# Performance work log

Hardware: AMD Instinct MI355X
Metric: run time of the kernel (lower is better)

The kernel has to match this reference:

```python
import jax, jax.numpy as jnp
import numpy as np

B, M, P, A, T = 32, 128, 20, 32, 32
H = 32   # embed_size / local hidden
E = 64   # local_hidden_dim = 2*H, global attention embed dim


def setup_inputs() -> dict:
    key = jax.random.key(0)
    ks = jax.random.split(key, 10)
    def w(k, shape, fan):
        return jax.random.normal(k, shape, jnp.float32) / np.float32(np.sqrt(fan))
    z = lambda *s: jnp.zeros(s, jnp.float32)
    o = lambda *s: jnp.ones(s, jnp.float32)
    return {
        "map_states": jax.random.normal(ks[0], (B, M, P, 16), jnp.float32),
        "agent_states": jax.random.normal(ks[1], (B, A, T, 4), jnp.float32),
        "m_W1": w(ks[2], (16, H), 16), "m_b1": z(H), "m_g1": o(H), "m_be1": z(H),
        "m_W2": w(ks[3], (H, H), H),   "m_b2": z(H), "m_g2": o(H), "m_be2": z(H),
        "a_W1": w(ks[4], (4, H), 4),   "a_b1": z(H), "a_g1": o(H), "a_be1": z(H),
        "a_W2": w(ks[5], (H, H), H),   "a_b2": z(H), "a_g2": o(H), "a_be2": z(H),
        # stacked attention params: index 0 = a2m, 1 = agent(self), 2 = m2a
        "att_Wq": w(ks[6], (3, E, E), E), "att_bq": z(3, E),
        "att_Wk": w(ks[7], (3, E, E), E), "att_bk": z(3, E),
        "att_Wv": w(ks[8], (3, E, E), E), "att_bv": z(3, E),
        "att_Wo": w(ks[9], (3, E, E), E), "att_bo": z(3, E),
    }


def _mlp(x, W, b, g, be):
    # Linear -> LayerNorm -> ReLU
    h = x @ W + b
    mu = jnp.mean(h, axis=-1, keepdims=True)
    var = jnp.var(h, axis=-1, keepdims=True)
    h = (h - mu) / jnp.sqrt(var + 1e-5) * g + be
    return jax.nn.relu(h)


def _local_graph(x, p1, p2):
    # x: [B, N, P, F] -> [B, N, 2H]
    e = _mlp(_mlp(x, *p1), *p2)                       # [B,N,P,H]
    n = e.shape[2]
    # faithful "max excluding self": max_j (e[j] - 10000*[j==i])
    mask = -10000.0 * jnp.eye(n, dtype=e.dtype)       # [Pi,Pj]
    nb = jnp.max(e[:, :, None, :, :] + mask[None, None, :, :, None], axis=3)  # [B,N,P,H]
    e = jnp.concatenate([e, nb], axis=-1)             # [B,N,P,2H]
    return jnp.max(e, axis=2)                          # [B,N,2H]


def _mha(q, k, v, Wq, bq, Wk, bk, Wv, bv, Wo, bo):
    # single-head attention, batch_first
    d = q.shape[-1]
    Q = q @ Wq + bq
    K = k @ Wk + bk
    V = v @ Wv + bv
    scores = jnp.einsum('bqd,bkd->bqk', Q, K) / jnp.sqrt(jnp.asarray(d, Q.dtype))
    attn = jax.nn.softmax(scores, axis=-1)
    return jnp.einsum('bqk,bkd->bqd', attn, V) @ Wo + bo


def reference(map_states, agent_states,
              m_W1, m_b1, m_g1, m_be1, m_W2, m_b2, m_g2, m_be2,
              a_W1, a_b1, a_g1, a_be1, a_W2, a_b2, a_g2, a_be2,
              att_Wq, att_bq, att_Wk, att_bk, att_Wv, att_bv, att_Wo, att_bo):
    map_emb = _local_graph(map_states, (m_W1, m_b1, m_g1, m_be1), (m_W2, m_b2, m_g2, m_be2))      # [B,M,E]
    agent_emb = _local_graph(agent_states, (a_W1, a_b1, a_g1, a_be1), (a_W2, a_b2, a_g2, a_be2))  # [B,A,E]

    target = agent_emb[:, :1]                                       # [B,1,E]
    kv = jnp.concatenate([target, map_emb], axis=1)                 # [B,M+1,E]
    a2m = _mha(map_emb, kv, kv, att_Wq[0], att_bq[0], att_Wk[0], att_bk[0],
               att_Wv[0], att_bv[0], att_Wo[0], att_bo[0])
    map_emb = map_emb + a2m
    t_a = _mha(target, target, target, att_Wq[1], att_bq[1], att_Wk[1], att_bk[1],
               att_Wv[1], att_bv[1], att_Wo[1], att_bo[1])
    t_m2a = _mha(target, map_emb, map_emb, att_Wq[2], att_bq[2], att_Wk[2], att_bk[2],
                 att_Wv[2], att_bv[2], att_Wo[2], att_bo[2])
    target = t_a + t_m2a                                            # [B,1,E]
    # pack (target_agent_embedding, map_embedding) into one array [B, M+1, E]
    return jnp.concatenate([target, map_emb], axis=1)
```

## Files before the change

kernel.cpp:

```cpp
#include <hip/hip_runtime.h>

#define BB 32
#define MM 128
#define PP 20
#define AA 32
#define TT 32
#define HH 32
#define EE 64

__device__ __forceinline__ float4 matvec64(const float* __restrict__ W,
                                           const float* __restrict__ xrow,
                                           int s, int t)
{
    const float4* __restrict__ Wv = (const float4*)W;
    const float4* __restrict__ xv = (const float4*)xrow;
    float4 acc = make_float4(0.f, 0.f, 0.f, 0.f);
#pragma unroll
    for (int ii = 0; ii < 4; ++ii) {
        const float4 xx = xv[s * 4 + ii];
        const int ib = s * 16 + ii * 4;
        const float4 w0 = Wv[(ib + 0) * 16 + t];
        const float4 w1 = Wv[(ib + 1) * 16 + t];
        const float4 w2 = Wv[(ib + 2) * 16 + t];
        const float4 w3 = Wv[(ib + 3) * 16 + t];
        acc.x = fmaf(xx.x, w0.x, acc.x); acc.y = fmaf(xx.x, w0.y, acc.y);
        acc.z = fmaf(xx.x, w0.z, acc.z); acc.w = fmaf(xx.x, w0.w, acc.w);
        acc.x = fmaf(xx.y, w1.x, acc.x); acc.y = fmaf(xx.y, w1.y, acc.y);
        acc.z = fmaf(xx.y, w1.z, acc.z); acc.w = fmaf(xx.y, w1.w, acc.w);
        acc.x = fmaf(xx.z, w2.x, acc.x); acc.y = fmaf(xx.z, w2.y, acc.y);
        acc.z = fmaf(xx.z, w2.z, acc.z); acc.w = fmaf(xx.z, w2.w, acc.w);
        acc.x = fmaf(xx.w, w3.x, acc.x); acc.y = fmaf(xx.w, w3.y, acc.y);
        acc.z = fmaf(xx.w, w3.z, acc.z); acc.w = fmaf(xx.w, w3.w, acc.w);
    }
    acc.x += __shfl_xor(acc.x, 16); acc.y += __shfl_xor(acc.y, 16);
    acc.z += __shfl_xor(acc.z, 16); acc.w += __shfl_xor(acc.w, 16);
    acc.x += __shfl_xor(acc.x, 32); acc.y += __shfl_xor(acc.y, 32);
    acc.z += __shfl_xor(acc.z, 32); acc.w += __shfl_xor(acc.w, 32);
    return acc;
}

template <int IN>
__device__ __forceinline__ void lg_body(const float* __restrict__ xg, int P,
                                        const float* __restrict__ W1, const float* __restrict__ b1,
                                        const float* __restrict__ g1, const float* __restrict__ be1,
                                        const float* __restrict__ W2, const float* __restrict__ b2,
                                        const float* __restrict__ g2, const float* __restrict__ be2,
                                        float* __restrict__ outRow)
{
    const int lane = threadIdx.x;
    const int sub  = lane >> 5;
    const int c    = lane & 31;

    float w1c[IN];
#pragma unroll
    for (int k = 0; k < IN; ++k) w1c[k] = W1[k * HH + c];
    float w2c[HH];
#pragma unroll
    for (int k = 0; k < HH; ++k) w2c[k] = W2[k * HH + c];
    const float b1c = b1[c], g1c = g1[c], be1c = be1[c];
    const float b2c = b2[c], g2c = g2[c], be2c = be2[c];

    float cmax = -1e30f;

    for (int p0 = 0; p0 < P; p0 += 2) {
        const int p = p0 + sub;
        const float* xp = xg + (long)p * IN;

        float h = b1c;
#pragma unroll
        for (int k = 0; k < IN; ++k) h = fmaf(xp[k], w1c[k], h);

        float sdot = h;
#pragma unroll
        for (int off = 16; off >= 1; off >>= 1) sdot += __shfl_xor(sdot, off, 32);
        const float mu = sdot * (1.0f / 32.0f);
        float d = h - mu;
        float sq = d * d;
#pragma unroll
        for (int off = 16; off >= 1; off >>= 1) sq += __shfl_xor(sq, off, 32);
        const float var = sq * (1.0f / 32.0f);
        float a = d * rsqrtf(var + 1e-5f) * g1c + be1c;
        a = fmaxf(a, 0.0f);

        float h2 = b2c;
#pragma unroll
        for (int k = 0; k < HH; ++k) h2 = fmaf(__shfl(a, k, 32), w2c[k], h2);

        float s2 = h2;
#pragma unroll
        for (int off = 16; off >= 1; off >>= 1) s2 += __shfl_xor(s2, off, 32);
        const float mu2 = s2 * (1.0f / 32.0f);
        float d2 = h2 - mu2;
        float sq2 = d2 * d2;
#pragma unroll
        for (int off = 16; off >= 1; off >>= 1) sq2 += __shfl_xor(sq2, off, 32);
        const float var2 = sq2 * (1.0f / 32.0f);
        float e = d2 * rsqrtf(var2 + 1e-5f) * g2c + be2c;
        e = fmaxf(e, 0.0f);

        cmax = fmaxf(cmax, e);
    }

    const float other = __shfl_xor(cmax, 32);
    cmax = fmaxf(cmax, other);
    if (sub == 0) {
        outRow[c]      = cmax;
        outRow[32 + c] = cmax;
    }
}

__global__ void lg_fused_kernel(const float* __restrict__ map_states,
                                const float* __restrict__ agent_states,
                                const float* __restrict__ mW1, const float* __restrict__ mb1,
                                const float* __restrict__ mg1, const float* __restrict__ mbe1,
                                const float* __restrict__ mW2, const float* __restrict__ mb2,
                                const float* __restrict__ mg2, const float* __restrict__ mbe2,
                                const float* __restrict__ aW1, const float* __restrict__ ab1,
                                const float* __restrict__ ag1, const float* __restrict__ abe1,
                                const float* __restrict__ aW2, const float* __restrict__ ab2,
                                const float* __restrict__ ag2, const float* __restrict__ abe2,
                                float* __restrict__ map_emb, float* __restrict__ target)
{
    const int g = blockIdx.x;
    if (g < BB * MM) {
        lg_body<16>(map_states + (long)g * PP * 16, PP,
                    mW1, mb1, mg1, mbe1, mW2, mb2, mg2, mbe2,
                    map_emb + (long)g * EE);
    } else {
        const int b = g - BB * MM;
        lg_body<4>(agent_states + (long)b * AA * TT * 4, TT,
                   aW1, ab1, ag1, abe1, aW2, ab2, ag2, abe2,
                   target + (long)b * EE);
    }
}

__global__ void kv_a2m_kernel(const float* __restrict__ map_emb,
                              const float* __restrict__ target,
                              const float* __restrict__ Wk, const float* __restrict__ bk,
                              const float* __restrict__ Wv, const float* __restrict__ bv,
                              float* __restrict__ Kb,
                              float* __restrict__ Vb)
{
    const int blk = blockIdx.x;
    const int b = blk / 129;
    const int r = blk % 129;
    const int lane = threadIdx.x;
    const int s = lane >> 4, t = lane & 15;

    __shared__ __align__(16) float xrow[EE];
    const float* src = (r == 0) ? (target + (long)b * EE)
                                : (map_emb + ((long)b * MM + (r - 1)) * EE);
    xrow[lane] = src[lane];
    __syncthreads();

    const float4 k4 = matvec64(Wk, xrow, s, t);
    const float4 v4 = matvec64(Wv, xrow, s, t);
    if (s == 0) {
        const float4 kb4 = ((const float4*)bk)[t];
        const float4 vb4 = ((const float4*)bv)[t];
        float4 ko, vo;
        ko.x = k4.x + kb4.x; ko.y = k4.y + kb4.y; ko.z = k4.z + kb4.z; ko.w = k4.w + kb4.w;
        vo.x = v4.x + vb4.x; vo.y = v4.y + vb4.y; vo.z = v4.z + vb4.z; vo.w = v4.w + vb4.w;
        ((float4*)(Kb + ((long)b * 129 + r) * EE))[t] = ko;
        ((float4*)(Vb + ((long)b * 129 + r) * EE))[t] = vo;
    }
}

__global__ void attn_fused_kernel(const float* __restrict__ map_emb,
                                  const float* __restrict__ Kb,
                                  const float* __restrict__ Vb,
                                  const float* __restrict__ Wq, const float* __restrict__ bq,
                                  const float* __restrict__ Wo, const float* __restrict__ bo,
                                  const float* __restrict__ Wk2, const float* __restrict__ bk2,
                                  const float* __restrict__ Wv2, const float* __restrict__ bv2,
                                  float* __restrict__ K2,
                                  float* __restrict__ V2,
                                  float* __restrict__ out)
{
    const int blk  = blockIdx.x;
    const int b    = blk >> 7;
    const int q    = blk & 127;
    const int lane = threadIdx.x;
    const int s = lane >> 4, t = lane & 15;

    __shared__ __align__(16) float xrow[EE];
    __shared__ __align__(16) float sc[132];
    __shared__ __align__(16) float av[EE];
    __shared__ __align__(16) float resrow[EE];

    xrow[lane] = map_emb[((long)b * MM + q) * EE + lane];
    __syncthreads();

    float4 q4 = matvec64(Wq, xrow, s, t);
    {
        const float4 bq4 = ((const float4*)bq)[t];
        q4.x = (q4.x + bq4.x) * 0.125f;
        q4.y = (q4.y + bq4.y) * 0.125f;
        q4.z = (q4.z + bq4.z) * 0.125f;
        q4.w = (q4.w + bq4.w) * 0.125f;
    }

    const float* Kbase = Kb + (long)b * 129 * EE;
    float mx = -1e30f;
#pragma unroll 4
    for (int it = 0; it < 33; ++it) {
        const int j = it * 4 + s;
        const bool valid = (j < 129);
        float p = 0.0f;
        if (valid) {
            const float4 k4 = ((const float4*)(Kbase + (long)j * EE))[t];
            p = q4.x * k4.x + q4.y * k4.y + q4.z * k4.z + q4.w * k4.w;
        }
        p += __shfl_xor(p, 1); p += __shfl_xor(p, 2);
        p += __shfl_xor(p, 4); p += __shfl_xor(p, 8);
        if (valid) {
            mx = fmaxf(mx, p);
            if (t == 0) sc[j] = p;
        }
    }
#pragma unroll
    for (int off = 32; off >= 1; off >>= 1) mx = fmaxf(mx, __shfl_xor(mx, off));
    __syncthreads();

    float sum = 0.0f;
    for (int j = lane; j < 129; j += 64) {
        const float e = __expf(sc[j] - mx);
        sc[j] = e;
        sum += e;
    }
#pragma unroll
    for (int off = 32; off >= 1; off >>= 1) sum += __shfl_xor(sum, off);
    const float inv = 1.0f / sum;
    __syncthreads();

    const float* Vbase = Vb + (long)b * 129 * EE;
    float acc = 0.0f;
#pragma unroll 4
    for (int j0 = 0; j0 < 128; j0 += 4) {
        const float4 s4 = *(const float4*)&sc[j0];
        acc = fmaf(s4.x, Vbase[(long)(j0 + 0) * EE + lane], acc);
        acc = fmaf(s4.y, Vbase[(long)(j0 + 1) * EE + lane], acc);
        acc = fmaf(s4.z, Vbase[(long)(j0 + 2) * EE + lane], acc);
        acc = fmaf(s4.w, Vbase[(long)(j0 + 3) * EE + lane], acc);
    }
    acc = fmaf(sc[128], Vbase[(long)128 * EE + lane], acc);
    acc *= inv;
    av[lane] = acc;
    __syncthreads();

    const float4 o4 = matvec64(Wo, av, s, t);
    const float4 bo4 = ((const float4*)bo)[t];
    const float4 x4 = ((const float4*)xrow)[t];
    float4 res;
    res.x = o4.x + bo4.x + x4.x;
    res.y = o4.y + bo4.y + x4.y;
    res.z = o4.z + bo4.z + x4.z;
    res.w = o4.w + bo4.w + x4.w;
    if (s == 0) {
        ((float4*)(out + ((long)b * 129 + 1 + q) * EE))[t] = res;
        ((float4*)resrow)[t] = res;
    }
    __syncthreads();

    const float4 k4 = matvec64(Wk2, resrow, s, t);
    const float4 v4 = matvec64(Wv2, resrow, s, t);
    if (s == 0) {
        const float4 kb4 = ((const float4*)bk2)[t];
        const float4 vb4 = ((const float4*)bv2)[t];
        float4 ko, vo;
        ko.x = k4.x + kb4.x; ko.y = k4.y + kb4.y; ko.z = k4.z + kb4.z; ko.w = k4.w + kb4.w;
        vo.x = v4.x + vb4.x; vo.y = v4.y + vb4.y; vo.z = v4.z + vb4.z; vo.w = v4.w + vb4.w;
        ((float4*)(K2 + ((long)b * MM + q) * EE))[t] = ko;
        ((float4*)(V2 + ((long)b * MM + q) * EE))[t] = vo;
    }
}

__global__ void target_kernel(const float* __restrict__ target,
                              const float* __restrict__ K2, const float* __restrict__ V2,
                              const float* __restrict__ Wq2, const float* __restrict__ bq2,
                              const float* __restrict__ Wo2, const float* __restrict__ bo2,
                              const float* __restrict__ Wv1, const float* __restrict__ bv1,
                              const float* __restrict__ Wo1, const float* __restrict__ bo1,
                              float* __restrict__ out)
{
    const int b    = blockIdx.x;
    const int lane = threadIdx.x;
    const int s = lane >> 4, t = lane & 15;

    __shared__ __align__(16) float trow[EE];
    __shared__ __align__(16) float tmp[EE];
    __shared__ __align__(16) float sc[128];
    __shared__ __align__(16) float av[EE];

    trow[lane] = target[(long)b * EE + lane];
    __syncthreads();

    const float4 v1 = matvec64(Wv1, trow, s, t);
    if (s == 0) {
        const float4 bv4 = ((const float4*)bv1)[t];
        float4 w; w.x = v1.x + bv4.x; w.y = v1.y + bv4.y; w.z = v1.z + bv4.z; w.w = v1.w + bv4.w;
        ((float4*)tmp)[t] = w;
    }
    __syncthreads();
    float4 ta = matvec64(Wo1, tmp, s, t);
    {
        const float4 bo4 = ((const float4*)bo1)[t];
        ta.x += bo4.x; ta.y += bo4.y; ta.z += bo4.z; ta.w += bo4.w;
    }

    float4 q4 = matvec64(Wq2, trow, s, t);
    {
        const float4 bq4 = ((const float4*)bq2)[t];
        q4.x = (q4.x + bq4.x) * 0.125f;
        q4.y = (q4.y + bq4.y) * 0.125f;
        q4.z = (q4.z + bq4.z) * 0.125f;
        q4.w = (q4.w + bq4.w) * 0.125f;
    }

    const float* Kbase = K2 + (long)b * MM * EE;
    float mx = -1e30f;
#pragma unroll 4
    for (int it = 0; it < 32; ++it) {
        const int j = it * 4 + s;
        const float4 k4 = ((const float4*)(Kbase + (long)j * EE))[t];
        float p = q4.x * k4.x + q4.y * k4.y + q4.z * k4.z + q4.w * k4.w;
        p += __shfl_xor(p, 1); p += __shfl_xor(p, 2);
        p += __shfl_xor(p, 4); p += __shfl_xor(p, 8);
        mx = fmaxf(mx, p);
        if (t == 0) sc[j] = p;
    }
#pragma unroll
    for (int off = 32; off >= 1; off >>= 1) mx = fmaxf(mx, __shfl_xor(mx, off));
    __syncthreads();

    float sum = 0.0f;
#pragma unroll
    for (int j = lane; j < MM; j += 64) {
        const float e = __expf(sc[j] - mx);
        sc[j] = e;
        sum += e;
    }
#pragma unroll
    for (int off = 32; off >= 1; off >>= 1) sum += __shfl_xor(sum, off);
    const float inv = 1.0f / sum;
    __syncthreads();

    const float* Vbase = V2 + (long)b * MM * EE;
    float acc = 0.0f;
#pragma unroll 4
    for (int j0 = 0; j0 < 128; j0 += 4) {
        const float4 s4 = *(const float4*)&sc[j0];
        acc = fmaf(s4.x, Vbase[(long)(j0 + 0) * EE + lane], acc);
        acc = fmaf(s4.y, Vbase[(long)(j0 + 1) * EE + lane], acc);
        acc = fmaf(s4.z, Vbase[(long)(j0 + 2) * EE + lane], acc);
        acc = fmaf(s4.w, Vbase[(long)(j0 + 3) * EE + lane], acc);
    }
    acc *= inv;
    av[lane] = acc;
    __syncthreads();

    const float4 o4 = matvec64(Wo2, av, s, t);
    if (s == 0) {
        const float4 bo4 = ((const float4*)bo2)[t];
        float4 r;
        r.x = ta.x + o4.x + bo4.x;
        r.y = ta.y + o4.y + bo4.y;
        r.z = ta.z + o4.z + bo4.z;
        r.w = ta.w + o4.w + bo4.w;
        ((float4*)(out + (long)b * 129 * EE))[t] = r;
    }
}

extern "C" void kernel_launch(void* const* d_in, const int* in_sizes, int n_in,
                              void* d_out, int out_size, void* d_ws, size_t ws_size,
                              hipStream_t stream)
{
    const float* map_states   = (const float*)d_in[0];
    const float* agent_states = (const float*)d_in[1];
    const float* m_W1 = (const float*)d_in[2];
    const float* m_b1 = (const float*)d_in[3];
    const float* m_g1 = (const float*)d_in[4];
    const float* m_be1 = (const float*)d_in[5];
    const float* m_W2 = (const float*)d_in[6];
    const float* m_b2 = (const float*)d_in[7];
    const float* m_g2 = (const float*)d_in[8];
    const float* m_be2 = (const float*)d_in[9];
    const float* a_W1 = (const float*)d_in[10];
    const float* a_b1 = (const float*)d_in[11];
    const float* a_g1 = (const float*)d_in[12];
    const float* a_be1 = (const float*)d_in[13];
    const float* a_W2 = (const float*)d_in[14];
    const float* a_b2 = (const float*)d_in[15];
    const float* a_g2 = (const float*)d_in[16];
    const float* a_be2 = (const float*)d_in[17];
    const float* att_Wq = (const float*)d_in[18];
    const float* att_bq = (const float*)d_in[19];
    const float* att_Wk = (const float*)d_in[20];
    const float* att_bk = (const float*)d_in[21];
    const float* att_Wv = (const float*)d_in[22];
    const float* att_bv = (const float*)d_in[23];
    const float* att_Wo = (const float*)d_in[24];
    const float* att_bo = (const float*)d_in[25];

    float* out = (float*)d_out;

    float* ws      = (float*)d_ws;
    float* map_emb = ws;
    float* target  = map_emb + BB * MM * EE;
    float* Kb      = target + BB * EE;
    float* Vb      = Kb + BB * 129 * EE;
    float* K2      = Vb + BB * 129 * EE;
    float* V2      = K2 + BB * MM * EE;

    const float* Wq0 = att_Wq + 0 * EE * EE; const float* bq0 = att_bq + 0 * EE;
    const float* Wk0 = att_Wk + 0 * EE * EE; const float* bk0 = att_bk + 0 * EE;
    const float* Wv0 = att_Wv + 0 * EE * EE; const float* bv0 = att_bv + 0 * EE;
    const float* Wo0 = att_Wo + 0 * EE * EE; const float* bo0 = att_bo + 0 * EE;
    const float* Wv1 = att_Wv + 1 * EE * EE; const float* bv1 = att_bv + 1 * EE;
    const float* Wo1 = att_Wo + 1 * EE * EE; const float* bo1 = att_bo + 1 * EE;
    const float* Wq2 = att_Wq + 2 * EE * EE; const float* bq2 = att_bq + 2 * EE;
    const float* Wk2 = att_Wk + 2 * EE * EE; const float* bk2 = att_bk + 2 * EE;
    const float* Wv2 = att_Wv + 2 * EE * EE; const float* bv2 = att_bv + 2 * EE;
    const float* Wo2 = att_Wo + 2 * EE * EE; const float* bo2 = att_bo + 2 * EE;

    hipLaunchKernelGGL(lg_fused_kernel, dim3(BB * MM + BB), dim3(64), 0, stream,
                       map_states, agent_states,
                       m_W1, m_b1, m_g1, m_be1, m_W2, m_b2, m_g2, m_be2,
                       a_W1, a_b1, a_g1, a_be1, a_W2, a_b2, a_g2, a_be2,
                       map_emb, target);

    hipLaunchKernelGGL(kv_a2m_kernel, dim3(BB * 129), dim3(64), 0, stream,
                       map_emb, target, Wk0, bk0, Wv0, bv0, Kb, Vb);

    hipLaunchKernelGGL(attn_fused_kernel, dim3(BB * MM), dim3(64), 0, stream,
                       map_emb, Kb, Vb, Wq0, bq0, Wo0, bo0,
                       Wk2, bk2, Wv2, bv2, K2, V2, out);

    hipLaunchKernelGGL(target_kernel, dim3(BB), dim3(64), 0, stream,
                       target, K2, V2, Wq2, bq2, Wo2, bo2, Wv1, bv1, Wo1, bo1, out);
}
```

Baseline: 196.0 us.

## Fuse local-graph encoder with a2m Q/K/V projections and widen blocks to 128 threads

Merges the local-graph embedding kernel with the K/V projection kernel, and moves the Q projection (pre-scaled by 1/sqrt(d)) out of the attention kernel, so each map/agent row's Q, K and V are computed right after its embedding in one launch. Blocks grow to 128 threads, handling 4 points per iteration with a shared-memory cross-wave max. The second MLP layer now broadcasts activations through LDS instead of 32 shuffles, and attention-value accumulations use four independent accumulators. This removes one kernel launch and the re-read of embeddings, at the cost of extra Q-buffer traffic and larger per-block shared memory and syncs.

```diff
diff --git a/kernel.cpp b/kernel.cpp
--- a/kernel.cpp
+++ b/kernel.cpp
@@ -40,16 +40,28 @@
 }
 
 template <int IN>
-__device__ __forceinline__ void lg_body(const float* __restrict__ xg, int P,
-                                        const float* __restrict__ W1, const float* __restrict__ b1,
-                                        const float* __restrict__ g1, const float* __restrict__ be1,
-                                        const float* __restrict__ W2, const float* __restrict__ b2,
-                                        const float* __restrict__ g2, const float* __restrict__ be2,
-                                        float* __restrict__ outRow)
-{
-    const int lane = threadIdx.x;
-    const int sub  = lane >> 5;
-    const int c    = lane & 31;
+__device__ __forceinline__ void lg_qkv_body(const float* __restrict__ xg, int P,
+                                            const float* __restrict__ W1, const float* __restrict__ b1,
+                                            const float* __restrict__ g1, const float* __restrict__ be1,
+                                            const float* __restrict__ W2, const float* __restrict__ b2,
+                                            const float* __restrict__ g2, const float* __restrict__ be2,
+                                            float* __restrict__ embRow,
+                                            const float* __restrict__ Wq, const float* __restrict__ bq,
+                                            const float* __restrict__ Wk, const float* __restrict__ bk,
+                                            const float* __restrict__ Wv, const float* __restrict__ bv,
+                                            float* __restrict__ Qrow,
+                                            float* __restrict__ Krow,
+                                            float* __restrict__ Vrow)
+{
+    const int tid  = threadIdx.x;
+    const int wave = tid >> 6;
+    const int lane = tid & 63;
+    const int sub  = tid >> 5;
+    const int c    = tid & 31;
+
+    __shared__ __align__(16) float aslot[4][32];
+    __shared__ __align__(16) float wmax[2][32];
+    __shared__ __align__(16) float xrow[EE];
 
     float w1c[IN];
 #pragma unroll
@@ -62,13 +74,27 @@
 
     float cmax = -1e30f;
 
-    for (int p0 = 0; p0 < P; p0 += 2) {
+    for (int p0 = 0; p0 < P; p0 += 4) {
         const int p = p0 + sub;
         const float* xp = xg + (long)p * IN;
 
         float h = b1c;
-#pragma unroll
-        for (int k = 0; k < IN; ++k) h = fmaf(xp[k], w1c[k], h);
+        if (IN == 16) {
+            const float4* xp4 = (const float4*)xp;
+            const float4 x0 = xp4[0], x1 = xp4[1], x2 = xp4[2], x3 = xp4[3];
+            h = fmaf(x0.x, w1c[0], h);  h = fmaf(x0.y, w1c[1], h);
+            h = fmaf(x0.z, w1c[2], h);  h = fmaf(x0.w, w1c[3], h);
+            h = fmaf(x1.x, w1c[4], h);  h = fmaf(x1.y, w1c[5], h);
+            h = fmaf(x1.z, w1c[6], h);  h = fmaf(x1.w, w1c[7], h);
+            h = fmaf(x2.x, w1c[8], h);  h = fmaf(x2.y, w1c[9], h);
+            h = fmaf(x2.z, w1c[10], h); h = fmaf(x2.w, w1c[11], h);
+            h = fmaf(x3.x, w1c[12], h); h = fmaf(x3.y, w1c[13], h);
+            h = fmaf(x3.z, w1c[14], h); h = fmaf(x3.w, w1c[15], h);
+        } else {
+            const float4 x0 = *(const float4*)xp;
+            h = fmaf(x0.x, w1c[0], h); h = fmaf(x0.y, w1c[1], h);
+            h = fmaf(x0.z, w1c[2], h); h = fmaf(x0.w, w1c[3], h);
+        }
 
         float sdot = h;
 #pragma unroll
@@ -82,9 +108,17 @@
         float a = d * rsqrtf(var + 1e-5f) * g1c + be1c;
         a = fmaxf(a, 0.0f);
 
+        aslot[sub][c] = a;
+        const float4* av4 = (const float4*)aslot[sub];
         float h2 = b2c;
 #pragma unroll
-        for (int k = 0; k < HH; ++k) h2 = fmaf(__shfl(a, k, 32), w2c[k], h2);
+        for (int j = 0; j < 8; ++j) {
+            const float4 aa = av4[j];
+            h2 = fmaf(aa.x, w2c[4 * j + 0], h2);
+            h2 = fmaf(aa.y, w2c[4 * j + 1], h2);
+            h2 = fmaf(aa.z, w2c[4 * j + 2], h2);
+            h2 = fmaf(aa.w, w2c[4 * j + 3], h2);
+        }
 
         float s2 = h2;
 #pragma unroll
@@ -101,75 +135,98 @@
         cmax = fmaxf(cmax, e);
     }
 
-    const float other = __shfl_xor(cmax, 32);
-    cmax = fmaxf(cmax, other);
-    if (sub == 0) {
-        outRow[c]      = cmax;
-        outRow[32 + c] = cmax;
-    }
-}
-
-__global__ void lg_fused_kernel(const float* __restrict__ map_states,
-                                const float* __restrict__ agent_states,
-                                const float* __restrict__ mW1, const float* __restrict__ mb1,
-                                const float* __restrict__ mg1, const float* __restrict__ mbe1,
-                                const float* __restrict__ mW2, const float* __restrict__ mb2,
-                                const float* __restrict__ mg2, const float* __restrict__ mbe2,
-                                const float* __restrict__ aW1, const float* __restrict__ ab1,
-                                const float* __restrict__ ag1, const float* __restrict__ abe1,
-                                const float* __restrict__ aW2, const float* __restrict__ ab2,
-                                const float* __restrict__ ag2, const float* __restrict__ abe2,
-                                float* __restrict__ map_emb, float* __restrict__ target)
+    cmax = fmaxf(cmax, __shfl_xor(cmax, 32));
+    if (lane < 32) wmax[wave][lane] = cmax;
+    __syncthreads();
+
+    if (tid < 32) {
+        const float fin = fmaxf(wmax[0][tid], wmax[1][tid]);
+        xrow[tid]      = fin;
+        xrow[tid + 32] = fin;
+        embRow[tid]      = fin;
+        embRow[tid + 32] = fin;
+    }
+    __syncthreads();
+
+    const int s = lane >> 4, t = lane & 15;
+    if (wave == 0) {
+        if (Qrow) {
+            float4 q4 = matvec64(Wq, xrow, s, t);
+            if (s == 0) {
+                const float4 bq4 = ((const float4*)bq)[t];
+                float4 qo;
+                qo.x = (q4.x + bq4.x) * 0.125f;
+                qo.y = (q4.y + bq4.y) * 0.125f;
+                qo.z = (q4.z + bq4.z) * 0.125f;
+                qo.w = (q4.w + bq4.w) * 0.125f;
+                ((float4*)Qrow)[t] = qo;
+            }
+        }
+        float4 k4 = matvec64(Wk, xrow, s, t);
+        if (s == 0) {
+            const float4 kb4 = ((const float4*)bk)[t];
+            float4 ko;
+            ko.x = k4.x + kb4.x; ko.y = k4.y + kb4.y;
+            ko.z = k4.z + kb4.z; ko.w = k4.w + kb4.w;
+            ((float4*)Krow)[t] = ko;
+        }
+    } else {
+        float4 v4 = matvec64(Wv, xrow, s, t);
+        if (s == 0) {
+            const float4 vb4 = ((const float4*)bv)[t];
+            float4 vo;
+            vo.x = v4.x + vb4.x; vo.y = v4.y + vb4.y;
+            vo.z = v4.z + vb4.z; vo.w = v4.w + vb4.w;
+            ((float4*)Vrow)[t] = vo;
+        }
+    }
+}
+
+__global__ void lg_qkv_kernel(const float* __restrict__ map_states,
+                              const float* __restrict__ agent_states,
+                              const float* __restrict__ mW1, const float* __restrict__ mb1,
+                              const float* __restrict__ mg1, const float* __restrict__ mbe1,
+                              const float* __restrict__ mW2, const float* __restrict__ mb2,
+                              const float* __restrict__ mg2, const float* __restrict__ mbe2,
+                              const float* __restrict__ aW1, const float* __restrict__ ab1,
+                              const float* __restrict__ ag1, const float* __restrict__ abe1,
+                              const float* __restrict__ aW2, const float* __restrict__ ab2,
+                              const float* __restrict__ ag2, const float* __restrict__ abe2,
+                              const float* __restrict__ Wq, const float* __restrict__ bq,
+                              const float* __restrict__ Wk, const float* __restrict__ bk,
+                              const float* __restrict__ Wv, const float* __restrict__ bv,
+                              float* __restrict__ map_emb,
+                              float* __restrict__ target,
+                              float* __restrict__ Qb,
+                              float* __restrict__ Kb,
+                              float* __restrict__ Vb)
 {
     const int g = blockIdx.x;
     if (g < BB * MM) {
-        lg_body<16>(map_states + (long)g * PP * 16, PP,
-                    mW1, mb1, mg1, mbe1, mW2, mb2, mg2, mbe2,
-                    map_emb + (long)g * EE);
+        const int b = g >> 7, m = g & 127;
+        lg_qkv_body<16>(map_states + (long)g * PP * 16, PP,
+                        mW1, mb1, mg1, mbe1, mW2, mb2, mg2, mbe2,
+                        map_emb + (long)g * EE,
+                        Wq, bq, Wk, bk, Wv, bv,
+                        Qb + (long)g * EE,
+                        Kb + ((long)b * 129 + 1 + m) * EE,
+                        Vb + ((long)b * 129 + 1 + m) * EE);
     } else {
         const int b = g - BB * MM;
-        lg_body<4>(agent_states + (long)b * AA * TT * 4, TT,
-                   aW1, ab1, ag1, abe1, aW2, ab2, ag2, abe2,
-                   target + (long)b * EE);
-    }
-}
-
-__global__ void kv_a2m_kernel(const float* __restrict__ map_emb,
-                              const float* __restrict__ target,
-                              const float* __restrict__ Wk, const float* __restrict__ bk,
-                              const float* __restrict__ Wv, const float* __restrict__ bv,
-                              float* __restrict__ Kb,
-                              float* __restrict__ Vb)
-{
-    const int blk = blockIdx.x;
-    const int b = blk / 129;
-    const int r = blk % 129;
-    const int lane = threadIdx.x;
-    const int s = lane >> 4, t = lane & 15;
-
-    __shared__ __align__(16) float xrow[EE];
-    const float* src = (r == 0) ? (target + (long)b * EE)
-                                : (map_emb + ((long)b * MM + (r - 1)) * EE);
-    xrow[lane] = src[lane];
-    __syncthreads();
-
-    const float4 k4 = matvec64(Wk, xrow, s, t);
-    const float4 v4 = matvec64(Wv, xrow, s, t);
-    if (s == 0) {
-        const float4 kb4 = ((const float4*)bk)[t];
-        const float4 vb4 = ((const float4*)bv)[t];
-        float4 ko, vo;
-        ko.x = k4.x + kb4.x; ko.y = k4.y + kb4.y; ko.z = k4.z + kb4.z; ko.w = k4.w + kb4.w;
-        vo.x = v4.x + vb4.x; vo.y = v4.y + vb4.y; vo.z = v4.z + vb4.z; vo.w = v4.w + vb4.w;
-        ((float4*)(Kb + ((long)b * 129 + r) * EE))[t] = ko;
-        ((float4*)(Vb + ((long)b * 129 + r) * EE))[t] = vo;
+        lg_qkv_body<4>(agent_states + (long)b * AA * TT * 4, TT,
+                       aW1, ab1, ag1, abe1, aW2, ab2, ag2, abe2,
+                       target + (long)b * EE,
+                       Wq, bq, Wk, bk, Wv, bv,
+                       nullptr,
+                       Kb + (long)b * 129 * EE,
+                       Vb + (long)b * 129 * EE);
     }
 }
 
 __global__ void attn_fused_kernel(const float* __restrict__ map_emb,
+                                  const float* __restrict__ Qb,
                                   const float* __restrict__ Kb,
                                   const float* __restrict__ Vb,
-                                  const float* __restrict__ Wq, const float* __restrict__ bq,
                                   const float* __restrict__ Wo, const float* __restrict__ bo,
                                   const float* __restrict__ Wk2, const float* __restrict__ bk2,
                                   const float* __restrict__ Wv2, const float* __restrict__ bv2,
@@ -183,22 +240,11 @@
     const int lane = threadIdx.x;
     const int s = lane >> 4, t = lane & 15;
 
-    __shared__ __align__(16) float xrow[EE];
     __shared__ __align__(16) float sc[132];
     __shared__ __align__(16) float av[EE];
     __shared__ __align__(16) float resrow[EE];
 
-    xrow[lane] = map_emb[((long)b * MM + q) * EE + lane];
-    __syncthreads();
-
-    float4 q4 = matvec64(Wq, xrow, s, t);
-    {
-        const float4 bq4 = ((const float4*)bq)[t];
-        q4.x = (q4.x + bq4.x) * 0.125f;
-        q4.y = (q4.y + bq4.y) * 0.125f;
-        q4.z = (q4.z + bq4.z) * 0.125f;
-        q4.w = (q4.w + bq4.w) * 0.125f;
-    }
+    const float4 q4 = ((const float4*)(Qb + ((long)b * MM + q) * EE))[t];
 
     const float* Kbase = Kb + (long)b * 129 * EE;
     float mx = -1e30f;
@@ -234,23 +280,23 @@
     __syncthreads();
 
     const float* Vbase = Vb + (long)b * 129 * EE;
-    float acc = 0.0f;
+    float a0 = 0.f, a1 = 0.f, a2 = 0.f, a3 = 0.f;
 #pragma unroll 4
     for (int j0 = 0; j0 < 128; j0 += 4) {
         const float4 s4 = *(const float4*)&sc[j0];
-        acc = fmaf(s4.x, Vbase[(long)(j0 + 0) * EE + lane], acc);
-        acc = fmaf(s4.y, Vbase[(long)(j0 + 1) * EE + lane], acc);
-        acc = fmaf(s4.z, Vbase[(long)(j0 + 2) * EE + lane], acc);
-        acc = fmaf(s4.w, Vbase[(long)(j0 + 3) * EE + lane], acc);
-    }
-    acc = fmaf(sc[128], Vbase[(long)128 * EE + lane], acc);
-    acc *= inv;
+        a0 = fmaf(s4.x, Vbase[(long)(j0 + 0) * EE + lane], a0);
+        a1 = fmaf(s4.y, Vbase[(long)(j0 + 1) * EE + lane], a1);
+        a2 = fmaf(s4.z, Vbase[(long)(j0 + 2) * EE + lane], a2);
+        a3 = fmaf(s4.w, Vbase[(long)(j0 + 3) * EE + lane], a3);
+    }
+    a0 = fmaf(sc[128], Vbase[(long)128 * EE + lane], a0);
+    const float acc = ((a0 + a1) + (a2 + a3)) * inv;
     av[lane] = acc;
     __syncthreads();
 
     const float4 o4 = matvec64(Wo, av, s, t);
     const float4 bo4 = ((const float4*)bo)[t];
-    const float4 x4 = ((const float4*)xrow)[t];
+    const float4 x4 = ((const float4*)(map_emb + ((long)b * MM + q) * EE))[t];
     float4 res;
     res.x = o4.x + bo4.x + x4.x;
     res.y = o4.y + bo4.y + x4.y;
@@ -346,17 +392,16 @@
     __syncthreads();
 
     const float* Vbase = V2 + (long)b * MM * EE;
-    float acc = 0.0f;
+    float a0 = 0.f, a1 = 0.f, a2 = 0.f, a3 = 0.f;
 #pragma unroll 4
     for (int j0 = 0; j0 < 128; j0 += 4) {
         const float4 s4 = *(const float4*)&sc[j0];
-        acc = fmaf(s4.x, Vbase[(long)(j0 + 0) * EE + lane], acc);
-        acc = fmaf(s4.y, Vbase[(long)(j0 + 1) * EE + lane], acc);
-        acc = fmaf(s4.z, Vbase[(long)(j0 + 2) * EE + lane], acc);
-        acc = fmaf(s4.w, Vbase[(long)(j0 + 3) * EE + lane], acc);
-    }
-    acc *= inv;
-    av[lane] = acc;
+        a0 = fmaf(s4.x, Vbase[(long)(j0 + 0) * EE + lane], a0);
+        a1 = fmaf(s4.y, Vbase[(long)(j0 + 1) * EE + lane], a1);
+        a2 = fmaf(s4.z, Vbase[(long)(j0 + 2) * EE + lane], a2);
+        a3 = fmaf(s4.w, Vbase[(long)(j0 + 3) * EE + lane], a3);
+    }
+    av[lane] = ((a0 + a1) + (a2 + a3)) * inv;
     __syncthreads();
 
     const float4 o4 = matvec64(Wo2, av, s, t);
@@ -407,7 +452,8 @@
     float* ws      = (float*)d_ws;
     float* map_emb = ws;
     float* target  = map_emb + BB * MM * EE;
-    float* Kb      = target + BB * EE;
+    float* Qb      = target + BB * EE;
+    float* Kb      = Qb + BB * MM * EE;
     float* Vb      = Kb + BB * 129 * EE;
     float* K2      = Vb + BB * 129 * EE;
     float* V2      = K2 + BB * MM * EE;
@@ -423,17 +469,15 @@
     const float* Wv2 = att_Wv + 2 * EE * EE; const float* bv2 = att_bv + 2 * EE;
     const float* Wo2 = att_Wo + 2 * EE * EE; const float* bo2 = att_bo + 2 * EE;
 
-    hipLaunchKernelGGL(lg_fused_kernel, dim3(BB * MM + BB), dim3(64), 0, stream,
+    hipLaunchKernelGGL(lg_qkv_kernel, dim3(BB * MM + BB), dim3(128), 0, stream,
                        map_states, agent_states,
                        m_W1, m_b1, m_g1, m_be1, m_W2, m_b2, m_g2, m_be2,
                        a_W1, a_b1, a_g1, a_be1, a_W2, a_b2, a_g2, a_be2,
-                       map_emb, target);
-
-    hipLaunchKernelGGL(kv_a2m_kernel, dim3(BB * 129), dim3(64), 0, stream,
-                       map_emb, target, Wk0, bk0, Wv0, bv0, Kb, Vb);
+                       Wq0, bq0, Wk0, bk0, Wv0, bv0,
+                       map_emb, target, Qb, Kb, Vb);
 
     hipLaunchKernelGGL(attn_fused_kernel, dim3(BB * MM), dim3(64), 0, stream,
-                       map_emb, Kb, Vb, Wq0, bq0, Wo0, bo0,
+                       map_emb, Qb, Kb, Vb, Wo0, bo0,
                        Wk2, bk2, Wv2, bv2, K2, V2, out);
 
     hipLaunchKernelGGL(target_kernel, dim3(BB), dim3(64), 0, stream,
```

After: 184.2 us. -6.0%, faster.
